# Optimization experiments

Measured on AMD Instinct MI355X. Metric: run time of the kernel, lower is better.

Reference implementation:

```python
import jax, jax.numpy as jnp
import numpy as np

NUM_CLASSES = 2
TOP_K = 1500
CONF_THRESH = 0.01
NMS_THRESH = 0.2
VAR0, VAR1 = 0.1, 0.2  # cfg['variance']


def setup_inputs() -> dict:
    key = jax.random.key(0)
    k1, k2, k3 = jax.random.split(key, 3)
    B, P = 32, 76800
    loc_data = jax.random.normal(k1, (B, P, 4), jnp.float32)
    conf_data = jax.random.uniform(k2, (B * P, NUM_CLASSES), jnp.float32)
    prior_data = jax.random.uniform(k3, (P, 4), jnp.float32)
    return {"loc_data": loc_data, "conf_data": conf_data, "prior_data": prior_data}


def _decode(loc, priors):
    # loc, priors: [P,4]; SSD box decode with variances
    cxcy = priors[:, :2] + loc[:, :2] * VAR0 * priors[:, 2:]
    wh = priors[:, 2:] * jnp.exp(loc[:, 2:] * VAR1)
    x1y1 = cxcy - wh * 0.5
    return jnp.concatenate([x1y1, x1y1 + wh], axis=-1)  # [P,4] (x1,y1,x2,y2)


def _nms_per_class(scores, boxes):
    # scores: [P], boxes: [P,4] -> [TOP_K,5] packed (score,x1,y1,x2,y2)
    s = jnp.where(scores > CONF_THRESH, scores, -jnp.inf)
    sk, idx = jax.lax.top_k(s, TOP_K)  # torch nms keeps only top_k candidates
    bk = boxes[idx]
    x1, y1, x2, y2 = bk[:, 0], bk[:, 1], bk[:, 2], bk[:, 3]
    area = (x2 - x1) * (y2 - y1)
    iota = jnp.arange(TOP_K)

    def step(active, i):
        # greedy NMS over score-descending candidates
        xx1 = jnp.maximum(x1, x1[i]); yy1 = jnp.maximum(y1, y1[i])
        xx2 = jnp.minimum(x2, x2[i]); yy2 = jnp.minimum(y2, y2[i])
        inter = jnp.maximum(xx2 - xx1, 0.0) * jnp.maximum(yy2 - yy1, 0.0)
        iou = inter / (area + area[i] - inter)
        kept = active[i]
        suppress = (iou > NMS_THRESH) & (iota != i)
        active = jnp.where(kept, active & ~suppress, active)
        return active, kept

    _, keep = jax.lax.scan(step, sk > -jnp.inf, iota)
    rows = jnp.where(keep[:, None], jnp.concatenate([sk[:, None], bk], axis=1), 0.0)
    # pack kept rows at the front (score-descending order), zeros after
    rank = jnp.cumsum(keep) - 1
    dest = jnp.where(keep, rank, TOP_K)  # dump non-kept into scratch slot
    return jnp.zeros((TOP_K + 1, 5), bk.dtype).at[dest].set(rows)[:TOP_K]


def reference(loc_data, conf_data, prior_data):
    B, P, _ = loc_data.shape
    conf = conf_data.reshape(B, P, NUM_CLASSES)
    decoded = jax.vmap(_decode, in_axes=(0, None))(loc_data, prior_data)  # [B,P,4]
    outs = []
    for cl in range(1, NUM_CLASSES):  # background class 0 stays zero
        outs.append(jax.vmap(_nms_per_class)(conf[:, :, cl], decoded))
    bg = jnp.zeros((B, 1, TOP_K, 5), decoded.dtype)
    return jnp.concatenate([bg, jnp.stack(outs, axis=1)], axis=1)  # [B,C,TOP_K,5]
```

## Files before the change

### kernel.cpp

```cpp
#include <hip/hip_runtime.h>
#include <stdint.h>

typedef unsigned long long u64;
typedef unsigned int u32;

#define NUM_B 32
#define NUM_P 76800
#define TOPK 1500
#define NBINS 2048
#define CAP 2048
#define NWORDS 24
#define NCHUNK 6
#define HSLICES 16
#define HCHUNK (NUM_P / HSLICES)

__device__ __forceinline__ u32 fbits(float f) { return __float_as_uint(f); }
__device__ __forceinline__ int binOf(float s) {
    int b = (int)(s * (float)NBINS);
    return (b > NBINS - 1) ? NBINS - 1 : b;
}
__device__ __forceinline__ u64 readlane64(u64 v, int l) {
    u32 lo = (u32)__builtin_amdgcn_readlane((int)(u32)(v & 0xffffffffu), l);
    u32 hi = (u32)__builtin_amdgcn_readlane((int)(u32)(v >> 32), l);
    return ((u64)hi << 32) | lo;
}

__global__ __launch_bounds__(256) void hist_kernel(const float4* __restrict__ conf4,
                                                   u32* __restrict__ hist,
                                                   u32* __restrict__ bpos) {
    int c = blockIdx.x, b = blockIdx.y, tid = threadIdx.x;
    if (tid < NBINS / HSLICES) bpos[(size_t)b * NBINS + c * (NBINS / HSLICES) + tid] = 0;
    __shared__ u32 h[NBINS];
    for (int i = tid; i < NBINS; i += 256) h[i] = 0;
    __syncthreads();
    const float4* base = conf4 + (size_t)b * (NUM_P / 2) + (size_t)c * (HCHUNK / 2);
    for (int i = tid; i < HCHUNK / 2; i += 256) {
        float4 v = base[i];
        if (v.y > 0.01f) atomicAdd(&h[binOf(v.y)], 1u);
        if (v.w > 0.01f) atomicAdd(&h[binOf(v.w)], 1u);
    }
    __syncthreads();
    u32* outp = hist + ((size_t)b * HSLICES + c) * NBINS;
    for (int i = tid; i < NBINS; i += 256) outp[i] = h[i];
}

__global__ void thresh_kernel(const u32* __restrict__ hist, int* __restrict__ tbin,
                              u32* __restrict__ binbase, u32* __restrict__ bincnt,
                              u32* __restrict__ ntotal) {
    int b = blockIdx.x;
    int tid = threadIdx.x;
    const u32* hb = hist + (size_t)b * HSLICES * NBINS;
    __shared__ u32 vals[256];
    __shared__ int s_min;
    u32 total = 0;
    for (int c = 0; c < NBINS / 256; ++c) {
        if (tid == 0) s_min = 256;
        int bin = NBINS - 1 - (c * 256 + tid);
        u32 v = 0;
#pragma unroll
        for (int s = 0; s < HSLICES; ++s) v += hb[(size_t)s * NBINS + bin];
        __syncthreads();
        vals[tid] = v;
        __syncthreads();
        for (int off = 1; off < 256; off <<= 1) {
            u32 add = (tid >= off) ? vals[tid - off] : 0;
            __syncthreads();
            vals[tid] += add;
            __syncthreads();
        }
        u32 cum = total + vals[tid];
        binbase[(size_t)b * NBINS + bin] = cum - v;
        bincnt [(size_t)b * NBINS + bin] = v;
        if (cum >= TOPK) atomicMin(&s_min, tid);
        __syncthreads();
        if (s_min < 256) {
            if (tid == 0) {
                tbin[b] = NBINS - 1 - (c * 256 + s_min);
                ntotal[b] = total + vals[s_min];
            }
            return;
        }
        total += vals[255];
    }
    if (tid == 0) { tbin[b] = 0; ntotal[b] = total; }
}

__global__ __launch_bounds__(256) void compact_kernel(
    const float4* __restrict__ conf4, const int* __restrict__ tbin,
    const u32* __restrict__ binbase, u32* __restrict__ bpos,
    u64* __restrict__ keys) {
    int b = blockIdx.y;
    int tid = threadIdx.x;
    int f4 = blockIdx.x * 256 + tid;
    float4 c = conf4[(size_t)b * (NUM_P / 2) + f4];
    int tb = tbin[b];
    int p0 = f4 * 2, p1 = p0 + 1;

    int b0 = binOf(c.y);
    if (c.y > 0.01f && b0 >= tb) {
        u32 slot = atomicAdd(&bpos[(size_t)b * NBINS + b0], 1u);
        u32 pos = binbase[(size_t)b * NBINS + b0] + slot;
        if (pos < CAP) keys[(size_t)b * CAP + pos] = ((u64)fbits(c.y) << 32) | (u32)(~p0);
    }
    int b1 = binOf(c.w);
    if (c.w > 0.01f && b1 >= tb) {
        u32 slot = atomicAdd(&bpos[(size_t)b * NBINS + b1], 1u);
        u32 pos = binbase[(size_t)b * NBINS + b1] + slot;
        if (pos < CAP) keys[(size_t)b * CAP + pos] = ((u64)fbits(c.w) << 32) | (u32)(~p1);
    }
}

__global__ __launch_bounds__(256) void rank_decode_kernel(
    const u64* __restrict__ keys, const u32* __restrict__ binbase,
    const u32* __restrict__ bincnt, const u32* __restrict__ ntotal,
    const float* __restrict__ loc, const float* __restrict__ prior,
    float* __restrict__ sscore, float* __restrict__ sbox) {
#pragma clang fp contract(off)
    int b = blockIdx.y;
    int g = blockIdx.x * 256 + threadIdx.x;
    int n = (int)min(ntotal[b], (u32)CAP);
    if (g >= n) return;
    const u64* kb = keys + (size_t)b * CAP;
    u64 mykey = kb[g];
    float sc = __uint_as_float((u32)(mykey >> 32));
    int bn = binOf(sc);
    u32 start = binbase[(size_t)b * NBINS + bn];
    u32 end = start + bincnt[(size_t)b * NBINS + bn];
    if (end > (u32)n) end = (u32)n;
    u32 rank = start;
#pragma unroll 4
    for (u32 j = start; j < end; ++j) rank += (kb[j] > mykey) ? 1u : 0u;

    if (rank < TOPK) {
        u32 pidx = ~(u32)mykey;
        const float* lp = &loc[((size_t)b * NUM_P + pidx) * 4];
        const float* pp = &prior[(size_t)pidx * 4];
        float lx = lp[0], ly = lp[1], lw = lp[2], lh = lp[3];
        float pcx = pp[0], pcy = pp[1], pw = pp[2], ph = pp[3];
        float cx = pcx + (lx * 0.1f) * pw;
        float cy = pcy + (ly * 0.1f) * ph;
        float w  = pw * expf(lw * 0.2f);
        float h  = ph * expf(lh * 0.2f);
        float x1 = cx - w * 0.5f;
        float y1 = cy - h * 0.5f;
        float x2 = x1 + w;
        float y2 = y1 + h;
        sscore[(size_t)b * TOPK + rank] = sc;
        float* bx = &sbox[((size_t)b * TOPK + rank) * 4];
        bx[0] = x1; bx[1] = y1; bx[2] = x2; bx[3] = y2;
    }
}

__global__ __launch_bounds__(256) void mask_kernel(
    const float* __restrict__ sbox, u64* __restrict__ mask) {
#pragma clang fp contract(off)
    int w = blockIdx.x, c = blockIdx.y, b = blockIdx.z, tid = threadIdx.x;
    int i = c * 256 + tid;
    if ((w * 64 + 63) <= (c * 256)) return;
    __shared__ float4 cbox[64];
    __shared__ float car[64];
    if (tid < 64) {
        int j = w * 64 + tid;
        float4 bx = make_float4(0.f, 0.f, 0.f, 0.f);
        if (j < TOPK) bx = ((const float4*)sbox)[(size_t)b * TOPK + j];
        cbox[tid] = bx;
        car[tid] = (bx.z - bx.x) * (bx.w - bx.y);
    }
    __syncthreads();
    if (i < TOPK && (w * 64 + 63) > i) {
        const double MID = 0.5 * ((double)__uint_as_float(0x3E4CCCCDu) +
                                  (double)__uint_as_float(0x3E4CCCCEu));
        const float4 bx = ((const float4*)sbox)[(size_t)b * TOPK + i];
        float x1i = bx.x, y1i = bx.y, x2i = bx.z, y2i = bx.w;
        float ai = (x2i - x1i) * (y2i - y1i);
        u64 jmask = (i < w * 64) ? ~0ULL : (~0ULL << (i - w * 64 + 1));
        u64 m = 0;
        for (int j2 = 0; j2 < 64; ++j2) {
            float4 cb = cbox[j2];
            float xx1 = fmaxf(cb.x, x1i);
            float yy1 = fmaxf(cb.y, y1i);
            float xx2 = fminf(cb.z, x2i);
            float yy2 = fminf(cb.w, y2i);
            float iw = fmaxf(xx2 - xx1, 0.0f);
            float ih = fmaxf(yy2 - yy1, 0.0f);
            float inter = iw * ih;
            float denom = (car[j2] + ai) - inter;
            if ((double)inter >= MID * (double)denom) m |= (1ULL << j2);
        }
        m &= jmask;
        mask[((size_t)b * NWORDS + w) * TOPK + i] = m;
    }
}

__global__ __launch_bounds__(256) void sweep_kernel(
    const u64* __restrict__ mask, const float* __restrict__ sscore,
    const float* __restrict__ sbox, float* __restrict__ out) {
    int b = blockIdx.x, tid = threadIdx.x;
    int lane = tid & 63, wid = tid >> 6;

    const u64* mbase = mask + (size_t)b * NWORDS * TOPK;

    __shared__ u64 rowbuf[3][NWORDS][65];
    __shared__ u64 aw[NWORDS];
    __shared__ u32 pfx[NWORDS + 1];

    u64 act = 0;
    u64 sv[8];
    if (wid == 0) {
        for (int c = 0; c < NWORDS; ++c) {
            int r = c * 64 + lane;
            bool v = (r < TOPK) && (sscore[(size_t)b * TOPK + r] > 0.0f);
            u64 m = __ballot(v);
            if (lane == c) act = m;
        }
    } else {
        int w0 = (wid - 1) * 8;
#pragma unroll
        for (int t = 0; t < 2; ++t) {
            u64 tmp[8];
#pragma unroll
            for (int k = 0; k < 8; ++k)
                tmp[k] = (w0 + k >= t) ? mbase[(size_t)(w0 + k) * TOPK + t * 64 + lane] : 0ULL;
#pragma unroll
            for (int k = 0; k < 8; ++k)
                rowbuf[t][w0 + k][lane] = tmp[k];
        }
        {
            int rr = 2 * 64 + lane;
#pragma unroll
            for (int k = 0; k < 8; ++k)
                sv[k] = (w0 + k >= 2) ? mbase[(size_t)(w0 + k) * TOPK + rr] : 0ULL;
        }
    }
    __syncthreads();

    for (int T = 0; T < NWORDS; ++T) {
        if (wid == 0) {
            u64 dreg = rowbuf[T % 3][T][lane];
            u64 actw = readlane64(act, T);
            u64 kept = 0, rem = actw;
            while (rem) {
                int i2 = __ffsll(rem) - 1;
                kept |= (1ULL << i2);
                rem &= rem - 1;
                rem &= ~readlane64(dreg, i2);
            }
            if (lane == T) act = kept;
            if (lane > T && lane < NWORDS) {
                u64 kb = kept;
                while (kb) {
                    int r = __ffsll(kb) - 1;
                    kb &= kb - 1;
                    act &= ~rowbuf[T % 3][lane][r];
                }
            }
        } else {
            int tw = T + 2;
            if (tw < NWORDS) {
                int w0 = (wid - 1) * 8;
#pragma unroll
                for (int k = 0; k < 8; ++k)
                    rowbuf[tw % 3][w0 + k][lane] = sv[k];
                int tn = T + 3;
                if (tn < NWORDS) {
                    int rr = tn * 64 + lane;
                    bool vr = rr < TOPK;
#pragma unroll
                    for (int k = 0; k < 8; ++k)
                        sv[k] = (vr && (w0 + k >= tn))
                                    ? mbase[(size_t)(w0 + k) * TOPK + rr] : 0ULL;
                }
            }
        }
        __syncthreads();
    }

    if (wid == 0 && lane < NWORDS) aw[lane] = act;
    {
        float4* pz = (float4*)(out + (size_t)b * 2 * TOPK * 5);
        float4 z4 = make_float4(0.f, 0.f, 0.f, 0.f);
        for (int t = tid; t < (2 * TOPK * 5) / 4; t += 256) pz[t] = z4;
    }
    __syncthreads();
    if (tid == 0) {
        u32 acc = 0;
        for (int wd = 0; wd < NWORDS; ++wd) { pfx[wd] = acc; acc += (u32)__popcll(aw[wd]); }
        pfx[NWORDS] = acc;
    }
    __syncthreads();
    for (int r = tid; r < TOPK; r += 256) {
        int wd = r >> 6;
        u64 word = aw[wd];
        if ((word >> (r & 63)) & 1ULL) {
            u32 rank = pfx[wd] + (u32)__popcll(word & ((1ULL << (r & 63)) - 1ULL));
            float sc = sscore[(size_t)b * TOPK + r];
            float4 bx = ((const float4*)sbox)[(size_t)b * TOPK + r];
            size_t base_o = (((size_t)b * 2 + 1) * TOPK + (size_t)rank) * 5;
            out[base_o + 0] = sc;
            out[base_o + 1] = bx.x;
            out[base_o + 2] = bx.y;
            out[base_o + 3] = bx.z;
            out[base_o + 4] = bx.w;
        }
    }
}

extern "C" void kernel_launch(void* const* d_in, const int* in_sizes, int n_in,
                              void* d_out, int out_size, void* d_ws, size_t ws_size,
                              hipStream_t stream) {
    const float* loc   = (const float*)d_in[0];
    const float* conf  = (const float*)d_in[1];
    const float* prior = (const float*)d_in[2];
    float* out = (float*)d_out;
    char* ws = (char*)d_ws;

    u64* mask_buf = (u64*)(ws + 0);
    u32* hist     = (u32*)(ws + 0);
    u32* binbase  = (u32*)(ws + 4194304);
    u32* bincnt   = (u32*)(ws + 4456448);
    u32* bpos     = (u32*)(ws + 4718592);
    u64* keys     = (u64*)(ws + 4980736);
    int* tbin     = (int*)(ws + 5505024);
    u32* ntotal   = (u32*)(ws + 5505152);
    float* sscore = (float*)(ws + 9216000);
    float* sbox   = (float*)(ws + 9408000);

    hist_kernel<<<dim3(HSLICES, 32), 256, 0, stream>>>((const float4*)conf, hist, bpos);
    thresh_kernel<<<32, 256, 0, stream>>>(hist, tbin, binbase, bincnt, ntotal);
    compact_kernel<<<dim3(150, 32), 256, 0, stream>>>((const float4*)conf, tbin, binbase,
                                                      bpos, keys);
    rank_decode_kernel<<<dim3(CAP / 256, 32), 256, 0, stream>>>(keys, binbase, bincnt,
                                                                ntotal, loc, prior,
                                                                sscore, sbox);
    mask_kernel<<<dim3(NWORDS, NCHUNK, 32), 256, 0, stream>>>(sbox, mask_buf);
    sweep_kernel<<<32, 256, 0, stream>>>(mask_buf, sscore, sbox, out);
}
```

Baseline: 178.5 us.

## Stage top-bin candidates in histogram pass, warp-scan threshold, branchless mask OR

```diff
diff --git a/kernel.cpp b/kernel.cpp
--- a/kernel.cpp
+++ b/kernel.cpp
@@ -13,6 +13,8 @@
 #define NCHUNK 6
 #define HSLICES 16
 #define HCHUNK (NUM_P / HSLICES)
+#define PB 1984
+#define SCAP 512
 
 __device__ __forceinline__ u32 fbits(float f) { return __float_as_uint(f); }
 __device__ __forceinline__ int binOf(float s) {
@@ -27,21 +29,47 @@
 
 __global__ __launch_bounds__(256) void hist_kernel(const float4* __restrict__ conf4,
                                                    u32* __restrict__ hist,
-                                                   u32* __restrict__ bpos) {
+                                                   u32* __restrict__ bpos,
+                                                   u64* __restrict__ skey,
+                                                   u32* __restrict__ scnt) {
     int c = blockIdx.x, b = blockIdx.y, tid = threadIdx.x;
     if (tid < NBINS / HSLICES) bpos[(size_t)b * NBINS + c * (NBINS / HSLICES) + tid] = 0;
     __shared__ u32 h[NBINS];
+    __shared__ u64 stg[SCAP];
+    __shared__ u32 sc_s;
+    if (tid == 0) sc_s = 0;
     for (int i = tid; i < NBINS; i += 256) h[i] = 0;
     __syncthreads();
     const float4* base = conf4 + (size_t)b * (NUM_P / 2) + (size_t)c * (HCHUNK / 2);
+    int pbase = c * HCHUNK;
     for (int i = tid; i < HCHUNK / 2; i += 256) {
         float4 v = base[i];
-        if (v.y > 0.01f) atomicAdd(&h[binOf(v.y)], 1u);
-        if (v.w > 0.01f) atomicAdd(&h[binOf(v.w)], 1u);
+        int p0 = pbase + i * 2;
+        if (v.y > 0.01f) {
+            int bn = binOf(v.y);
+            atomicAdd(&h[bn], 1u);
+            if (bn >= PB) {
+                u32 s = atomicAdd(&sc_s, 1u);
+                if (s < SCAP) stg[s] = ((u64)fbits(v.y) << 32) | (u32)(~p0);
+            }
+        }
+        if (v.w > 0.01f) {
+            int bn = binOf(v.w);
+            atomicAdd(&h[bn], 1u);
+            if (bn >= PB) {
+                u32 s = atomicAdd(&sc_s, 1u);
+                if (s < SCAP) stg[s] = ((u64)fbits(v.w) << 32) | (u32)(~(p0 + 1));
+            }
+        }
     }
     __syncthreads();
     u32* outp = hist + ((size_t)b * HSLICES + c) * NBINS;
     for (int i = tid; i < NBINS; i += 256) outp[i] = h[i];
+    u32 n = sc_s;
+    if (tid == 0) scnt[b * HSLICES + c] = n;
+    u64* sk = skey + (size_t)(b * HSLICES + c) * SCAP;
+    u32 nn = (n < (u32)SCAP) ? n : (u32)SCAP;
+    for (u32 i = tid; i < nn; i += 256) sk[i] = stg[i];
 }
 
 __global__ void thresh_kernel(const u32* __restrict__ hist, int* __restrict__ tbin,
@@ -49,38 +77,41 @@
                               u32* __restrict__ ntotal) {
     int b = blockIdx.x;
     int tid = threadIdx.x;
+    int lane = tid & 63, wid = tid >> 6;
     const u32* hb = hist + (size_t)b * HSLICES * NBINS;
-    __shared__ u32 vals[256];
-    __shared__ int s_min;
+    __shared__ u32 wsum[4];
+    __shared__ int s_min[NBINS / 256];
+    if (tid < NBINS / 256) s_min[tid] = 256;
+    __syncthreads();
     u32 total = 0;
     for (int c = 0; c < NBINS / 256; ++c) {
-        if (tid == 0) s_min = 256;
         int bin = NBINS - 1 - (c * 256 + tid);
         u32 v = 0;
 #pragma unroll
         for (int s = 0; s < HSLICES; ++s) v += hb[(size_t)s * NBINS + bin];
+        u32 x = v;
+#pragma unroll
+        for (int off = 1; off < 64; off <<= 1) {
+            u32 y = __shfl_up(x, off, 64);
+            if (lane >= off) x += y;
+        }
+        if (lane == 63) wsum[wid] = x;
         __syncthreads();
-        vals[tid] = v;
-        __syncthreads();
-        for (int off = 1; off < 256; off <<= 1) {
-            u32 add = (tid >= off) ? vals[tid - off] : 0;
-            __syncthreads();
-            vals[tid] += add;
-            __syncthreads();
-        }
-        u32 cum = total + vals[tid];
+        u32 woff = 0;
+        for (int w2 = 0; w2 < wid; ++w2) woff += wsum[w2];
+        u32 csum = wsum[0] + wsum[1] + wsum[2] + wsum[3];
+        u32 incl = woff + x;
+        u32 cum = total + incl;
         binbase[(size_t)b * NBINS + bin] = cum - v;
         bincnt [(size_t)b * NBINS + bin] = v;
-        if (cum >= TOPK) atomicMin(&s_min, tid);
+        if (cum >= TOPK) atomicMin(&s_min[c], tid);
         __syncthreads();
-        if (s_min < 256) {
-            if (tid == 0) {
-                tbin[b] = NBINS - 1 - (c * 256 + s_min);
-                ntotal[b] = total + vals[s_min];
-            }
+        int sm = s_min[c];
+        if (sm < 256) {
+            if (tid == sm) { tbin[b] = bin; ntotal[b] = cum; }
             return;
         }
-        total += vals[255];
+        total += csum;
     }
     if (tid == 0) { tbin[b] = 0; ntotal[b] = total; }
 }
@@ -88,14 +119,36 @@
 __global__ __launch_bounds__(256) void compact_kernel(
     const float4* __restrict__ conf4, const int* __restrict__ tbin,
     const u32* __restrict__ binbase, u32* __restrict__ bpos,
-    u64* __restrict__ keys) {
+    u64* __restrict__ keys, const u64* __restrict__ skey,
+    const u32* __restrict__ scnt) {
     int b = blockIdx.y;
     int tid = threadIdx.x;
+    int tb = tbin[b];
+    if (tb >= PB) {
+        bool ovf = false;
+#pragma unroll
+        for (int s = 0; s < HSLICES; ++s) ovf |= (scnt[b * HSLICES + s] > (u32)SCAP);
+        if (!ovf) {
+            if (blockIdx.x >= HSLICES) return;
+            int sl = blockIdx.x;
+            u32 cnt = scnt[b * HSLICES + sl];
+            const u64* sk = skey + (size_t)(b * HSLICES + sl) * SCAP;
+            for (u32 i = tid; i < cnt; i += 256) {
+                u64 key = sk[i];
+                float sc = __uint_as_float((u32)(key >> 32));
+                int bn = binOf(sc);
+                if (bn >= tb) {
+                    u32 slot = atomicAdd(&bpos[(size_t)b * NBINS + bn], 1u);
+                    u32 pos = binbase[(size_t)b * NBINS + bn] + slot;
+                    if (pos < CAP) keys[(size_t)b * CAP + pos] = key;
+                }
+            }
+            return;
+        }
+    }
     int f4 = blockIdx.x * 256 + tid;
     float4 c = conf4[(size_t)b * (NUM_P / 2) + f4];
-    int tb = tbin[b];
     int p0 = f4 * 2, p1 = p0 + 1;
-
     int b0 = binOf(c.y);
     if (c.y > 0.01f && b0 >= tb) {
         u32 slot = atomicAdd(&bpos[(size_t)b * NBINS + b0], 1u);
@@ -247,11 +300,22 @@
             }
             if (lane == T) act = kept;
             if (lane > T && lane < NWORDS) {
-                u64 kb = kept;
-                while (kb) {
-                    int r = __ffsll(kb) - 1;
-                    kb &= kb - 1;
-                    act &= ~rowbuf[T % 3][lane][r];
+                const u64* rb = rowbuf[T % 3][lane];
+                if (__popcll(kept) > 4) {
+                    u64 acc = 0;
+#pragma unroll 16
+                    for (int j = 0; j < 64; ++j) {
+                        u64 sel = (u64)0 - ((kept >> j) & 1ULL);
+                        acc |= rb[j] & sel;
+                    }
+                    act &= ~acc;
+                } else {
+                    u64 kb = kept;
+                    while (kb) {
+                        int r = __ffsll(kb) - 1;
+                        kb &= kb - 1;
+                        act &= ~rb[r];
+                    }
                 }
             }
         } else {
@@ -322,13 +386,16 @@
     u64* keys     = (u64*)(ws + 4980736);
     int* tbin     = (int*)(ws + 5505024);
     u32* ntotal   = (u32*)(ws + 5505152);
+    u64* skey     = (u64*)(ws + 5505280);
+    u32* scnt     = (u32*)(ws + 7602432);
     float* sscore = (float*)(ws + 9216000);
     float* sbox   = (float*)(ws + 9408000);
 
-    hist_kernel<<<dim3(HSLICES, 32), 256, 0, stream>>>((const float4*)conf, hist, bpos);
+    hist_kernel<<<dim3(HSLICES, 32), 256, 0, stream>>>((const float4*)conf, hist, bpos,
+                                                       skey, scnt);
     thresh_kernel<<<32, 256, 0, stream>>>(hist, tbin, binbase, bincnt, ntotal);
     compact_kernel<<<dim3(150, 32), 256, 0, stream>>>((const float4*)conf, tbin, binbase,
-                                                      bpos, keys);
+                                                      bpos, keys, skey, scnt);
     rank_decode_kernel<<<dim3(CAP / 256, 32), 256, 0, stream>>>(keys, binbase, bincnt,
                                                                 ntotal, loc, prior,
                                                                 sscore, sbox);
```

Result: slower. 182.5 us (+2.2%).
